# Optimization experiments

Measured on AMD Instinct MI355X. Metric: run time of the kernel, lower is better.

## Reference

```python
import jax, jax.numpy as jnp
import numpy as np

N_GRAPHS = 512  # number of graphs in the batch
S2S_STEPS = 3   # Set2Set processing_steps


def segment_softmax(e, seg, num_seg):
    m = jax.ops.segment_max(e, seg, num_segments=num_seg)
    ex = jnp.exp(e - m[seg])
    s = jax.ops.segment_sum(ex, seg, num_segments=num_seg)
    return ex / s[seg]


def setup_inputs() -> dict:
    key = jax.random.key(0)
    ks = jax.random.split(key, 24)
    N, E, Fin, Fe, D = 30000, 480000, 25, 14, 256
    s = 0.05
    inp = {
        "x": jax.random.normal(ks[0], (N, Fin), jnp.float32),
        "edge_attr": jax.random.normal(ks[1], (E, Fe), jnp.float32),
        # lin0
        "W0": jax.random.normal(ks[2], (Fin, D), jnp.float32) * s,
        "b0": jnp.zeros((D,), jnp.float32),
        # DMPNN edge-message MLP: [x_src || e_attr] -> D -> D
        "Wm1": jax.random.normal(ks[3], (D + Fe, D), jnp.float32) * s,
        "bm1": jnp.zeros((D,), jnp.float32),
        "Wm2": jax.random.normal(ks[4], (D, D), jnp.float32) * s,
        "bm2": jnp.zeros((D,), jnp.float32),
        # node (root) update
        "Wr": jax.random.normal(ks[5], (D, D), jnp.float32) * s,
        "br": jnp.zeros((D,), jnp.float32),
        # Set2Set LSTM: input 2D -> hidden D
        "Wih": jax.random.normal(ks[6], (2 * D, 4 * D), jnp.float32) * s,
        "Whh": jax.random.normal(ks[7], (D, 4 * D), jnp.float32) * s,
        "bl": jnp.zeros((4 * D,), jnp.float32),
        # readout MLP
        "W1": jax.random.normal(ks[8], (2 * D, D), jnp.float32) * s,
        "b1": jnp.zeros((D,), jnp.float32),
        "W2": jax.random.normal(ks[9], (D, 1), jnp.float32) * s,
        "b2": jnp.zeros((1,), jnp.float32),
        "edge_index": jax.random.randint(ks[10], (2, E), 0, N, jnp.int32),
        "batch": jnp.sort(jax.random.randint(ks[11], (N,), 0, N_GRAPHS, jnp.int32)),
    }
    return inp


def reference(x, edge_attr, W0, b0, Wm1, bm1, Wm2, bm2, Wr, br,
              Wih, Whh, bl, W1, b1, W2, b2, edge_index, batch):
    N = x.shape[0]
    # lin0 + relu
    h0 = jax.nn.relu(x @ W0 + b0)  # [N, D]
    # DMPNNLayer2: edge-conditioned message, sum-aggregate, root update (eval: no dropout)
    src, dst = edge_index[0], edge_index[1]
    m = jax.nn.relu(jnp.concatenate([h0[src], edge_attr], axis=-1) @ Wm1 + bm1)  # [E, D]
    m = m @ Wm2 + bm2
    agg = jax.ops.segment_sum(m, dst, num_segments=N)  # [N, D]
    out = jax.nn.relu(h0 @ Wr + br + agg)  # relu in top-level forward, massage_depth=1
    # Set2Set pooling (processing_steps=3)
    D = out.shape[1]
    B = N_GRAPHS
    q_star = jnp.zeros((B, 2 * D), out.dtype)
    h = jnp.zeros((B, D), out.dtype)
    c = jnp.zeros((B, D), out.dtype)
    for _ in range(S2S_STEPS):
        gates = q_star @ Wih + h @ Whh + bl  # [B, 4D]
        i, f, g, o = jnp.split(gates, 4, axis=-1)
        c = jax.nn.sigmoid(f) * c + jax.nn.sigmoid(i) * jnp.tanh(g)
        h = jax.nn.sigmoid(o) * jnp.tanh(c)
        e = jnp.sum(out * h[batch], axis=-1)              # [N]
        a = segment_softmax(e, batch, B)                  # [N]
        r = jax.ops.segment_sum(a[:, None] * out, batch, num_segments=B)  # [B, D]
        q_star = jnp.concatenate([h, r], axis=-1)
    # readout (eval: dropout identity)
    y = jax.nn.relu(q_star @ W1 + b1)
    y = y @ W2 + b2
    return y.reshape(-1)
```

## Files before the change

kernel.cpp:

```cpp
#include <hip/hip_runtime.h>

typedef unsigned short u16;
typedef unsigned char u8;
typedef unsigned int u32;
using s16x8 = __attribute__((ext_vector_type(8))) short;
using f32x4 = __attribute__((ext_vector_type(4))) float;

#define DEV static __device__ __forceinline__

DEV float b2f(u16 u) { return __uint_as_float(((u32)u) << 16); }
DEV u16 f2bu(float f) {
    u32 u = __float_as_uint(f);
    u32 r = (u + 0x7FFFu + ((u >> 16) & 1u)) >> 16;
    return (u16)r;
}
DEV float sigm(float x) { return 1.0f / (1.0f + expf(-x)); }

DEV float ldv(const void* p, int i, int f32flag) {
    if (f32flag) return ((const float*)p)[i];
    return b2f(((const u16*)p)[i]);
}
DEV void stv(void* p, int i, float v, int f32flag) {
    if (f32flag) ((float*)p)[i] = v;
    else ((u16*)p)[i] = f2bu(v);
}

DEV int lower_bound(const int* b, int n, int v) {
    int lo = 0, hi = n;
    while (lo < hi) { int mid = (lo + hi) >> 1; if (b[mid] < v) lo = mid + 1; else hi = mid; }
    return lo;
}

__global__ void DMPNN_Change_678604832935_kernel(int* p) {
    if (p && threadIdx.x == 0 && blockIdx.x == 0) p[0] = 1;
}

__global__ void detect_kernel(const void* x, int* flag) {
    __shared__ int cnt[128];
    int tid = threadIdx.x;
    if (tid < 128) {
        u16 v = ((const u16*)x)[tid];
        int e = (v >> 7) & 0xFF;
        cnt[tid] = (e >= 100 && e <= 141) ? 1 : 0;
    }
    __syncthreads();
    if (tid == 0) {
        int s = 0;
        for (int i = 0; i < 128; ++i) s += cnt[i];
        flag[0] = (s < 110) ? 1 : 0;
    }
}

__global__ void fillv_kernel(void* out, const int* flag, float v) {
    int i = blockIdx.x * 256 + threadIdx.x;
    if (i < 512) stv(out, i, v, flag[0]);
}

__global__ void zero_kernel(float* p, int n) {
    int i = blockIdx.x * 256 + threadIdx.x;
    int stride = gridDim.x * 256;
    for (; i < n; i += stride) p[i] = 0.0f;
}

__global__ void hist_kernel(const int* __restrict__ eidx, u32* __restrict__ cnt) {
    int i = blockIdx.x * 256 + threadIdx.x;
    if (i < 480000) atomicAdd(&cnt[eidx[480000 + i]], 1u);
}

__global__ void scan1_kernel(const u32* __restrict__ cnt, u32* __restrict__ part) {
    __shared__ u32 s[256];
    int i = blockIdx.x * 256 + threadIdx.x;
    s[threadIdx.x] = (i < 30000) ? cnt[i] : 0u;
    __syncthreads();
    for (int st = 128; st > 0; st >>= 1) {
        if (threadIdx.x < st) s[threadIdx.x] += s[threadIdx.x + st];
        __syncthreads();
    }
    if (threadIdx.x == 0) part[blockIdx.x] = s[0];
}

__global__ void scan2_kernel(const u32* __restrict__ part, u32* __restrict__ pexcl, int nb) {
    if (threadIdx.x == 0 && blockIdx.x == 0) {
        u32 run = 0;
        for (int i = 0; i < nb; ++i) { pexcl[i] = run; run += part[i]; }
    }
}

__global__ void scan3_kernel(u32* __restrict__ cursor, const u32* __restrict__ pexcl) {
    __shared__ u32 s[256];
    int b = blockIdx.x, tid = threadIdx.x;
    int i = b * 256 + tid;
    u32 v = (i < 30000) ? cursor[i] : 0u;
    s[tid] = v;
    __syncthreads();
    for (int off = 1; off < 256; off <<= 1) {
        u32 t = (tid >= off) ? s[tid - off] : 0u;
        __syncthreads();
        s[tid] += t;
        __syncthreads();
    }
    u32 excl = s[tid] - v + pexcl[b];
    if (i < 30000) cursor[i] = excl;
}

__global__ void scatter_kernel(const int* __restrict__ eidx, u32* __restrict__ cursor,
                               u16* __restrict__ permLo, u8* __restrict__ permHi) {
    int i = blockIdx.x * 256 + threadIdx.x;
    if (i < 480000) {
        int d = eidx[480000 + i];
        u32 pos = atomicAdd(&cursor[d], 1u);
        permLo[pos] = (u16)(i & 0xFFFF);
        permHi[pos] = (u8)(i >> 16);
    }
}

__global__ void deg_kernel(const u32* __restrict__ cursor, float* __restrict__ degf) {
    int i = blockIdx.x * 256 + threadIdx.x;
    if (i < 30000) {
        u32 end = cursor[i];
        u32 beg = (i > 0) ? cursor[i - 1] : 0u;
        degf[i] = (float)(end - beg);
    }
}

__global__ void to_blocked(const void* src, int K, int ktiles, const int* flag,
                           u16* dst) {
    int idx = blockIdx.x * 256 + threadIdx.x;
    int total = ktiles * 4 * 256 * 8;
    if (idx >= total) return;
    int f32 = flag[0];
    int c = idx & 7;
    int n = (idx >> 3) & 255;
    int jk = idx >> 11;
    int j = jk & 3, kt = jk >> 2;
    int k = kt * 32 + j * 8 + c;
    u16 v = 0;
    if (k < K) v = f2bu(ldv(src, k * 256 + n, f32));
    dst[idx] = v;
}

__global__ void to_blocked2(const void* src1, int K1, const void* src2, int K2,
                            const int* flag, u16* dst) {
    int idx = blockIdx.x * 256 + threadIdx.x;
    int total = 24 * 4 * 1024 * 8;
    if (idx >= total) return;
    int f32 = flag[0];
    int c = idx & 7;
    int n = (idx >> 3) & 1023;
    int jk = idx >> 13;
    int j = jk & 3, kt = jk >> 2;
    int k = kt * 32 + j * 8 + c;
    u16 v = 0;
    if (k < K1) v = f2bu(ldv(src1, k * 1024 + n, f32));
    else if (k - K1 < K2) v = f2bu(ldv(src2, (k - K1) * 1024 + n, f32));
    dst[idx] = v;
}

__global__ __launch_bounds__(256) void lin0_kernel(const void* x, const void* W0,
                                                   const void* b0, const int* flag,
                                                   u16* h0b) {
    int f32 = flag[0];
    int n0 = blockIdx.x * 8, tid = threadIdx.x;
    __shared__ float xs[8][26];
    if (tid < 200) {
        int nn = tid / 25, k = tid % 25;
        xs[nn][k] = ldv(x, (n0 + nn) * 25 + k, f32);
    }
    __syncthreads();
    float wr[25];
    #pragma unroll
    for (int k = 0; k < 25; ++k) wr[k] = ldv(W0, k * 256 + tid, f32);
    float bias = ldv(b0, tid, f32);
    #pragma unroll
    for (int nn = 0; nn < 8; ++nn) {
        float a = bias;
        #pragma unroll
        for (int k = 0; k < 25; ++k) a += xs[nn][k] * wr[k];
        h0b[(n0 + nn) * 256 + tid] = f2bu(fmaxf(a, 0.0f));
    }
}

__global__ __launch_bounds__(256) void qgen_kernel(
    const u16* __restrict__ h0b, const u16* __restrict__ Wm1b,
    u16* __restrict__ Qb) {
    __shared__ __attribute__((aligned(16))) u16 As[64 * 264];
    const int tid = threadIdx.x;
    const int w = tid >> 6, lane = tid & 63, quad = lane >> 4, mrow = lane & 15;
    const int row0 = blockIdx.x * 64;
    const int colb = w * 64 + mrow;
    const int r = tid >> 2, sub = tid & 3;

    {
        int row = row0 + r;
        u16* arow = As + r * 264;
        #pragma unroll
        for (int j = 0; j < 8; ++j) {
            int c0 = sub * 64 + j * 8;
            s16x8 v = {0, 0, 0, 0, 0, 0, 0, 0};
            if (row < 30000) v = *(const s16x8*)(h0b + row * 256 + c0);
            *(s16x8*)(arow + c0) = v;
        }
    }
    __syncthreads();

    f32x4 acc[4][4];
    f32x4 fzero = {0.f, 0.f, 0.f, 0.f};
    #pragma unroll
    for (int mi = 0; mi < 4; ++mi)
        #pragma unroll
        for (int ni = 0; ni < 4; ++ni) acc[mi][ni] = fzero;

    for (int kt = 0; kt < 8; ++kt) {
        s16x8 af[4], bf[4];
        #pragma unroll
        for (int ni = 0; ni < 4; ++ni)
            bf[ni] = *(const s16x8*)(Wm1b + (((kt * 4 + quad) * 256) + colb + ni * 16) * 8);
        #pragma unroll
        for (int mi = 0; mi < 4; ++mi)
            af[mi] = *(const s16x8*)(As + (mi * 16 + mrow) * 264 + kt * 32 + quad * 8);
        #pragma unroll
        for (int mi = 0; mi < 4; ++mi)
            #pragma unroll
            for (int ni = 0; ni < 4; ++ni)
                acc[mi][ni] = __builtin_amdgcn_mfma_f32_16x16x32_bf16(af[mi], bf[ni], acc[mi][ni], 0, 0, 0);
    }

    #pragma unroll
    for (int mi = 0; mi < 4; ++mi)
        #pragma unroll
        for (int rg = 0; rg < 4; ++rg) {
            int row = row0 + mi * 16 + quad * 4 + rg;
            if (row >= 30000) continue;
            #pragma unroll
            for (int ni = 0; ni < 4; ++ni)
                Qb[row * 256 + colb + ni * 16] = f2bu(acc[mi][ni][rg]);
        }
}

#define MAXD 96
__global__ __launch_bounds__(256) void edge_agg_kernel(
    const u16* __restrict__ Qb, const void* __restrict__ eattr,
    const int* __restrict__ eidx,
    const u16* __restrict__ permLo, const u8* __restrict__ permHi,
    const u32* __restrict__ cursor,
    const void* __restrict__ Wm1, const void* __restrict__ bm1,
    const int* __restrict__ flag, float* __restrict__ aggP) {
    const int f32 = flag[0];
    const int n = blockIdx.x, tid = threadIdx.x;
    const int beg = (n > 0) ? (int)cursor[n - 1] : 0;
    const int end = (int)cursor[n];
    __shared__ int eids[MAXD];
    __shared__ int sorted_s[MAXD];
    __shared__ int srcs[MAXD];
    __shared__ float Es[MAXD][15];

    float wc[14];
    #pragma unroll
    for (int k = 0; k < 14; ++k) wc[k] = ldv(Wm1, (256 + k) * 256 + tid, f32);
    const float bm1c = ldv(bm1, tid, f32);

    float acc = 0.0f;
    for (int base = beg; base < end; base += MAXD) {
        int cnt = end - base; if (cnt > MAXD) cnt = MAXD;
        if (tid < cnt) {
            int si = base + tid;
            eids[tid] = (int)permLo[si] | ((int)permHi[si] << 16);
        }
        __syncthreads();
        if (tid < cnt) {
            int key = eids[tid], r = 0;
            for (int j = 0; j < cnt; ++j) r += (eids[j] < key);
            sorted_s[r] = key;
        }
        __syncthreads();
        if (tid < cnt) srcs[tid] = eidx[sorted_s[tid]];
        for (int idx = tid; idx < cnt * 14; idx += 256) {
            int i = idx / 14, k = idx - i * 14;
            Es[i][k] = ldv(eattr, sorted_s[i] * 14 + k, f32);
        }
        __syncthreads();
        for (int i = 0; i < cnt; ++i) {
            float q = b2f(Qb[srcs[i] * 256 + tid]);
            float et = bm1c;
            #pragma unroll
            for (int k = 0; k < 14; ++k) et += Es[i][k] * wc[k];
            acc += fmaxf(q + et, 0.0f);
        }
        __syncthreads();
    }
    aggP[n * 256 + tid] = acc;
}

__global__ __launch_bounds__(256) void edge_sorted_kernel(
    const u16* __restrict__ h0b, const void* __restrict__ eattr,
    const int* __restrict__ eidx,
    const u16* __restrict__ permLo, const u8* __restrict__ permHi,
    const u16* __restrict__ Wm1b,
    const void* __restrict__ bm1,
    const int* __restrict__ flag, float* __restrict__ aggP) {
    __shared__ __attribute__((aligned(16))) u16 As[64 * 296];
    __shared__ int dsh[64];
    const int f32 = flag[0];
    const int tid = threadIdx.x;
    const int w = tid >> 6, lane = tid & 63, quad = lane >> 4, mrow = lane & 15;
    const int eb0 = blockIdx.x * 64;
    const int colb = w * 64 + mrow;

    if (tid < 64) {
        int sj = eb0 + tid;
        int ee = (int)permLo[sj] | ((int)permHi[sj] << 16);
        dsh[tid] = eidx[480000 + ee];
    }
    {
        int r = tid >> 2, sub = tid & 3;
        int si = eb0 + r;
        int e = (int)permLo[si] | ((int)permHi[si] << 16);
        int src = eidx[e];
        const u16* hrow = h0b + src * 256;
        u16* arow = As + r * 296;
        #pragma unroll
        for (int j = 0; j < 8; ++j) {
            int c0 = sub * 64 + j * 8;
            *(s16x8*)(arow + c0) = *(const s16x8*)(hrow + c0);
        }
        if (sub == 0) {
            for (int c = 0; c < 14; ++c) arow[256 + c] = f2bu(ldv(eattr, e * 14 + c, f32));
            for (int c = 14; c < 40; ++c) arow[256 + c] = 0;
        }
    }
    __syncthreads();

    f32x4 acc[4][4];
    f32x4 fzero = {0.f, 0.f, 0.f, 0.f};
    #pragma unroll
    for (int mi = 0; mi < 4; ++mi)
        #pragma unroll
        for (int ni = 0; ni < 4; ++ni) acc[mi][ni] = fzero;

    for (int kt = 0; kt < 9; ++kt) {
        s16x8 af[4], bf[4];
        #pragma unroll
        for (int ni = 0; ni < 4; ++ni)
            bf[ni] = *(const s16x8*)(Wm1b + (((kt * 4 + quad) * 256) + colb + ni * 16) * 8);
        #pragma unroll
        for (int mi = 0; mi < 4; ++mi)
            af[mi] = *(const s16x8*)(As + (mi * 16 + mrow) * 296 + kt * 32 + quad * 8);
        #pragma unroll
        for (int mi = 0; mi < 4; ++mi)
            #pragma unroll
            for (int ni = 0; ni < 4; ++ni)
                acc[mi][ni] = __builtin_amdgcn_mfma_f32_16x16x32_bf16(af[mi], bf[ni], acc[mi][ni], 0, 0, 0);
    }

    float bm1c[4];
    #pragma unroll
    for (int ni = 0; ni < 4; ++ni) bm1c[ni] = ldv(bm1, colb + ni * 16, f32);
    __syncthreads();
    #pragma unroll
    for (int mi = 0; mi < 4; ++mi)
        #pragma unroll
        for (int ni = 0; ni < 4; ++ni)
            #pragma unroll
            for (int rg = 0; rg < 4; ++rg) {
                int row = mi * 16 + quad * 4 + rg;
                As[row * 296 + colb + ni * 16] = f2bu(fmaxf(acc[mi][ni][rg] + bm1c[ni], 0.0f));
            }
    __syncthreads();

    {
        int c = tid;
        float s = 0.0f;
        int cur = dsh[0];
        #pragma unroll 8
        for (int rr = 0; rr < 64; ++rr) {
            int d = dsh[rr];
            if (d != cur) { atomicAdd(&aggP[cur * 256 + c], s); s = 0.0f; cur = d; }
            s += b2f(As[rr * 296 + c]);
        }
        atomicAdd(&aggP[cur * 256 + c], s);
    }
}

__global__ __launch_bounds__(256) void node_dual_kernel(
    u16* __restrict__ h0b, const u16* __restrict__ Wrb, const u16* __restrict__ Wm2b,
    const void* __restrict__ br, const void* __restrict__ bm2,
    const float* __restrict__ aggP, const float* __restrict__ degf,
    const int* __restrict__ flag) {
    __shared__ __attribute__((aligned(16))) u16 As[64 * 264];
    const int f32 = flag[0];
    const int tid = threadIdx.x;
    const int w = tid >> 6, lane = tid & 63, quad = lane >> 4, mrow = lane & 15;
    const int row0 = blockIdx.x * 64;
    const int colb = w * 64 + mrow;
    const int r = tid >> 2, sub = tid & 3;

    {
        int row = row0 + r;
        u16* arow = As + r * 264;
        #pragma unroll
        for (int j = 0; j < 8; ++j) {
            int c0 = sub * 64 + j * 8;
            s16x8 v = {0, 0, 0, 0, 0, 0, 0, 0};
            if (row < 30000) v = *(const s16x8*)(h0b + row * 256 + c0);
            *(s16x8*)(arow + c0) = v;
        }
    }
    __syncthreads();

    f32x4 acc[4][4];
    f32x4 fzero = {0.f, 0.f, 0.f, 0.f};
    #pragma unroll
    for (int mi = 0; mi < 4; ++mi)
        #pragma unroll
        for (int ni = 0; ni < 4; ++ni) acc[mi][ni] = fzero;

    for (int kt = 0; kt < 8; ++kt) {
        s16x8 af[4], bf[4];
        #pragma unroll
        for (int ni = 0; ni < 4; ++ni)
            bf[ni] = *(const s16x8*)(Wrb + (((kt * 4 + quad) * 256) + colb + ni * 16) * 8);
        #pragma unroll
        for (int mi = 0; mi < 4; ++mi)
            af[mi] = *(const s16x8*)(As + (mi * 16 + mrow) * 264 + kt * 32 + quad * 8);
        #pragma unroll
        for (int mi = 0; mi < 4; ++mi)
            #pragma unroll
            for (int ni = 0; ni < 4; ++ni)
                acc[mi][ni] = __builtin_amdgcn_mfma_f32_16x16x32_bf16(af[mi], bf[ni], acc[mi][ni], 0, 0, 0);
    }
    __syncthreads();

    {
        int row = row0 + r;
        u16* arow = As + r * 264;
        #pragma unroll
        for (int j = 0; j < 8; ++j) {
            int c0 = sub * 64 + j * 8;
            s16x8 pk = {0, 0, 0, 0, 0, 0, 0, 0};
            if (row < 30000) {
                f32x4 a = *(const f32x4*)(aggP + row * 256 + c0);
                f32x4 b = *(const f32x4*)(aggP + row * 256 + c0 + 4);
                pk[0] = (short)f2bu(a[0]); pk[1] = (short)f2bu(a[1]);
                pk[2] = (short)f2bu(a[2]); pk[3] = (short)f2bu(a[3]);
                pk[4] = (short)f2bu(b[0]); pk[5] = (short)f2bu(b[1]);
                pk[6] = (short)f2bu(b[2]); pk[7] = (short)f2bu(b[3]);
            }
            *(s16x8*)(arow + c0) = pk;
        }
    }
    __syncthreads();

    for (int kt = 0; kt < 8; ++kt) {
        s16x8 af[4], bf[4];
        #pragma unroll
        for (int ni = 0; ni < 4; ++ni)
            bf[ni] = *(const s16x8*)(Wm2b + (((kt * 4 + quad) * 256) + colb + ni * 16) * 8);
        #pragma unroll
        for (int mi = 0; mi < 4; ++mi)
            af[mi] = *(const s16x8*)(As + (mi * 16 + mrow) * 264 + kt * 32 + quad * 8);
        #pragma unroll
        for (int mi = 0; mi < 4; ++mi)
            #pragma unroll
            for (int ni = 0; ni < 4; ++ni)
                acc[mi][ni] = __builtin_amdgcn_mfma_f32_16x16x32_bf16(af[mi], bf[ni], acc[mi][ni], 0, 0, 0);
    }

    #pragma unroll
    for (int mi = 0; mi < 4; ++mi)
        #pragma unroll
        for (int rg = 0; rg < 4; ++rg) {
            int row = row0 + mi * 16 + quad * 4 + rg;
            if (row >= 30000) continue;
            float dg = degf[row];
            #pragma unroll
            for (int ni = 0; ni < 4; ++ni) {
                int col = colb + ni * 16;
                float v = acc[mi][ni][rg] + ldv(br, col, f32) + dg * ldv(bm2, col, f32);
                h0b[row * 256 + col] = f2bu(fmaxf(v, 0.0f));
            }
        }
}

__global__ __launch_bounds__(256) void gates_mfma_kernel(
    const u16* __restrict__ Abuf, const u16* __restrict__ Wcatb,
    float* __restrict__ G) {
    const int tid = threadIdx.x;
    const int w = tid >> 6, lane = tid & 63, quad = lane >> 4, mrow = lane & 15;
    const int row0 = blockIdx.x * 64;
    const int col = blockIdx.y * 64 + w * 16 + mrow;

    f32x4 acc[4];
    f32x4 fzero = {0.f, 0.f, 0.f, 0.f};
    #pragma unroll
    for (int mi = 0; mi < 4; ++mi) acc[mi] = fzero;

    for (int kt = 0; kt < 24; ++kt) {
        s16x8 bfv = *(const s16x8*)(Wcatb + (((kt * 4 + quad) * 1024) + col) * 8);
        s16x8 af[4];
        #pragma unroll
        for (int mi = 0; mi < 4; ++mi)
            af[mi] = *(const s16x8*)(Abuf + (row0 + mi * 16 + mrow) * 768 + kt * 32 + quad * 8);
        #pragma unroll
        for (int mi = 0; mi < 4; ++mi)
            acc[mi] = __builtin_amdgcn_mfma_f32_16x16x32_bf16(af[mi], bfv, acc[mi], 0, 0, 0);
    }

    #pragma unroll
    for (int mi = 0; mi < 4; ++mi)
        #pragma unroll
        for (int rg = 0; rg < 4; ++rg)
            G[(row0 + mi * 16 + quad * 4 + rg) * 1024 + col] = acc[mi][rg];
}

__global__ __launch_bounds__(256) void lstm_kernel(const float* G, const void* bl,
                                                   const int* flag,
                                                   float* Cst, float* Hst,
                                                   u16* Abuf) {
    int f32 = flag[0];
    int b = blockIdx.x, d = threadIdx.x;
    float gi = G[b * 1024 + d]       + ldv(bl, d, f32);
    float gf = G[b * 1024 + 256 + d] + ldv(bl, 256 + d, f32);
    float gg = G[b * 1024 + 512 + d] + ldv(bl, 512 + d, f32);
    float go = G[b * 1024 + 768 + d] + ldv(bl, 768 + d, f32);
    float c = Cst[b * 256 + d];
    c = sigm(gf) * c + sigm(gi) * tanhf(gg);
    Cst[b * 256 + d] = c;
    float h = sigm(go) * tanhf(c);
    Hst[b * 256 + d] = h;
    u16 hb = f2bu(h);
    Abuf[b * 768 + d] = hb;
    Abuf[b * 768 + 512 + d] = hb;
}

__global__ __launch_bounds__(256) void e_kernel(const u16* outb, const float* Hst,
                                                const int* batch, float* ebuf) {
    __shared__ float part[8][33];
    int tid = threadIdx.x;
    int g8 = tid >> 5, l = tid & 31;
    for (int n0 = blockIdx.x * 8; n0 < 30000; n0 += gridDim.x * 8) {
        int n = n0 + g8;
        float p = 0.0f;
        if (n < 30000) {
            int g = batch[n];
            const u16* orow = outb + n * 256 + l * 8;
            const float* hrow = Hst + g * 256 + l * 8;
            #pragma unroll
            for (int c = 0; c < 8; ++c) p += b2f(orow[c]) * hrow[c];
        }
        part[g8][l] = p;
        __syncthreads();
        if (tid < 8) {
            int n2 = n0 + tid;
            if (n2 < 30000) {
                float s = 0.0f;
                #pragma unroll
                for (int i = 0; i < 32; ++i) s += part[tid][i];
                ebuf[n2] = s;
            }
        }
        __syncthreads();
    }
}

__global__ __launch_bounds__(256) void graph_kernel(const float* ebuf, const u16* outb,
                                                    const int* batch, float* Rst,
                                                    u16* Abuf) {
    int b = blockIdx.x, tid = threadIdx.x;
    int n0 = lower_bound(batch, 30000, b);
    int n1 = lower_bound(batch, 30000, b + 1);
    __shared__ float red[256];
    __shared__ float pb[256];
    float r_out = 0.0f;
    if (n1 > n0) {
        float m = -1e30f;
        for (int n = n0 + tid; n < n1; n += 256) m = fmaxf(m, ebuf[n]);
        red[tid] = m; __syncthreads();
        for (int s = 128; s > 0; s >>= 1) { if (tid < s) red[tid] = fmaxf(red[tid], red[tid + s]); __syncthreads(); }
        m = red[0]; __syncthreads();
        float sl = 0.0f;
        for (int n = n0 + tid; n < n1; n += 256) sl += expf(ebuf[n] - m);
        red[tid] = sl; __syncthreads();
        for (int s = 128; s > 0; s >>= 1) { if (tid < s) red[tid] += red[tid + s]; __syncthreads(); }
        float ssum = red[0]; __syncthreads();
        float acc = 0.0f;
        for (int c0 = n0; c0 < n1; c0 += 256) {
            int nn = n1 - c0; if (nn > 256) nn = 256;
            __syncthreads();
            if (tid < nn) pb[tid] = expf(ebuf[c0 + tid] - m);
            __syncthreads();
            for (int i = 0; i < nn; ++i) acc += pb[i] * b2f(outb[(c0 + i) * 256 + tid]);
        }
        r_out = acc / ssum;
    }
    Rst[b * 256 + tid] = r_out;
    Abuf[b * 768 + 256 + tid] = f2bu(r_out);
}

__global__ __launch_bounds__(256) void readout_kernel(const float* Hst, const float* Rst,
                                                      const void* W1, const void* b1,
                                                      const void* W2, const void* b2,
                                                      const u16* nodeout, const float* aggP,
                                                      const int* flag, void* out) {
    int f32 = flag[0];
    int b = blockIdx.x, tid = threadIdx.x;
    __shared__ float qs[512];
    __shared__ float red[256];
    qs[tid] = Hst[b * 256 + tid];
    qs[256 + tid] = Rst[b * 256 + tid];
    __syncthreads();
    float a = ldv(b1, tid, f32);
    for (int k = 0; k < 512; ++k) a += qs[k] * ldv(W1, k * 256 + tid, f32);
    a = fmaxf(a, 0.0f) * ldv(W2, tid, f32);
    red[tid] = a; __syncthreads();
    for (int s = 128; s > 0; s >>= 1) { if (tid < s) red[tid] += red[tid + s]; __syncthreads(); }
    if (tid == 0) {
        float D = 0.0f;
        if (b == 0) {
            float s1 = 0.0f, s2 = 0.0f, s3 = 0.0f;
            for (int i = 0; i < 256; ++i) {
                s1 += fabsf(b2f(nodeout[i]));
                s2 += fabsf(aggP[i]);
                s3 += fabsf(Rst[i]);
            }
            if (s1 < 1e-3f) D += 100.0f;
            if (s2 < 1e-3f) D += 200.0f;
            if (s3 < 1e-6f) D += 400.0f;
        }
        stv(out, b, red[0] + ldv(b2, 0, f32) + D, f32);
    }
}

#define OFF_FLAG 0
#define OFF_HST  64
#define OFF_RST  524352
#define OFF_CST  1048640
#define OFF_PLO  64
#define OFF_PHI  960064
#define OFF_CUR  1440064
#define OFF_WREG 1572928
#define OFF_WM1B (OFF_WREG)
#define OFF_WM2B (OFF_WREG + 147456)
#define OFF_WRB  (OFF_WREG + 278528)
#define OFF_WCAT (OFF_WREG + 409600)
#define OFF_E    3670080
#define OFF_AGG  3790144
#define OFF_ABUF (OFF_AGG + 1048576)
#define OFF_G    (OFF_AGG + 4194304)
#define OFF_H0B  34510144
#define WS_NEEDED 49870144
#define OFF_Q    49870144
#define WS_FAST  (49870144 + 15360000)

extern "C" __attribute__((visibility("default")))
void kernel_launch(void* const* d_in, const int* in_sizes, int n_in,
                   void* d_out, int out_size, void* d_ws, size_t ws_size,
                   hipStream_t stream) {
    char* ws = (char*)d_ws;
    int*   flag   = (int*)(ws + OFF_FLAG);
    float* Hst    = (float*)(ws + OFF_HST);
    float* Rst    = (float*)(ws + OFF_RST);
    float* Cst    = (float*)(ws + OFF_CST);
    u16*   permLo = (u16*)(ws + OFF_PLO);
    u8*    permHi = (u8*)(ws + OFF_PHI);
    u32*   cursor = (u32*)(ws + OFF_CUR);
    u16*   Wm1b   = (u16*)(ws + OFF_WM1B);
    u16*   Wm2b   = (u16*)(ws + OFF_WM2B);
    u16*   Wrb    = (u16*)(ws + OFF_WRB);
    u16*   Wcatb  = (u16*)(ws + OFF_WCAT);
    float* ebuf   = (float*)(ws + OFF_E);
    u32*   part   = (u32*)(ws + OFF_E);
    u32*   pexcl  = (u32*)(ws + OFF_E + 512);
    float* degf   = (float*)(ws + OFF_E);
    float* aggP   = (float*)(ws + OFF_AGG);
    u16*   Abuf   = (u16*)(ws + OFF_ABUF);
    float* G      = (float*)(ws + OFF_G);
    u16*   h0b    = (u16*)(ws + OFF_H0B);
    u16*   Qb     = (u16*)(ws + OFF_Q);

    detect_kernel<<<1, 256, 0, stream>>>(d_in[0], flag);

    bool sizes_ok = (n_in == 19)
        && in_sizes[0] == 30000 * 25
        && in_sizes[1] == 480000 * 14
        && in_sizes[4] == 270 * 256
        && in_sizes[10] == 512 * 1024
        && in_sizes[17] == 2 * 480000
        && in_sizes[18] == 30000;
    if (!sizes_ok) { fillv_kernel<<<2, 256, 0, stream>>>(d_out, flag, 1600.0f); return; }
    if (ws_size < (size_t)WS_NEEDED) { fillv_kernel<<<2, 256, 0, stream>>>(d_out, flag, 800.0f); return; }
    const bool fast = (ws_size >= (size_t)WS_FAST);

    fillv_kernel<<<2, 256, 0, stream>>>(d_out, flag, 3.0f);
    DMPNN_Change_678604832935_kernel<<<1, 64, 0, stream>>>((int*)(ws + OFF_G));

    const void* x     = d_in[0];
    const void* eattr = d_in[1];
    const void* W0    = d_in[2];
    const void* b0    = d_in[3];
    const void* Wm1   = d_in[4];
    const void* bm1   = d_in[5];
    const void* Wm2   = d_in[6];
    const void* bm2   = d_in[7];
    const void* Wr    = d_in[8];
    const void* br    = d_in[9];
    const void* Wih   = d_in[10];
    const void* Whh   = d_in[11];
    const void* bl    = d_in[12];
    const void* W1    = d_in[13];
    const void* b1    = d_in[14];
    const void* W2    = d_in[15];
    const void* b2    = d_in[16];
    const int* eidx   = (const int*)d_in[17];
    const int* batch  = (const int*)d_in[18];

    to_blocked<<<288, 256, 0, stream>>>(Wm1, 270, 9, flag, Wm1b);
    to_blocked<<<256, 256, 0, stream>>>(Wm2, 256, 8, flag, Wm2b);
    to_blocked<<<256, 256, 0, stream>>>(Wr, 256, 8, flag, Wrb);
    to_blocked2<<<3072, 256, 0, stream>>>(Wih, 512, Whh, 256, flag, Wcatb);

    lin0_kernel<<<3750, 256, 0, stream>>>(x, W0, b0, flag, h0b);

    zero_kernel<<<30, 256, 0, stream>>>((float*)cursor, 30000);
    hist_kernel<<<1875, 256, 0, stream>>>(eidx, cursor);
    scan1_kernel<<<118, 256, 0, stream>>>(cursor, part);
    scan2_kernel<<<1, 64, 0, stream>>>(part, pexcl, 118);
    scan3_kernel<<<118, 256, 0, stream>>>(cursor, pexcl);
    scatter_kernel<<<1875, 256, 0, stream>>>(eidx, cursor, permLo, permHi);
    deg_kernel<<<118, 256, 0, stream>>>(cursor, degf);

    if (fast) {
        qgen_kernel<<<469, 256, 0, stream>>>(h0b, Wm1b, Qb);
        edge_agg_kernel<<<30000, 256, 0, stream>>>(Qb, eattr, eidx, permLo, permHi,
                                                   cursor, Wm1, bm1, flag, aggP);
    } else {
        zero_kernel<<<1024, 256, 0, stream>>>(aggP, 7680000);
        edge_sorted_kernel<<<7500, 256, 0, stream>>>(h0b, eattr, eidx, permLo, permHi,
                                                     Wm1b, bm1, flag, aggP);
    }
    node_dual_kernel<<<469, 256, 0, stream>>>(h0b, Wrb, Wm2b, br, bm2, aggP, degf, flag);

    zero_kernel<<<64, 256, 0, stream>>>(Cst, 131072);
    zero_kernel<<<64, 256, 0, stream>>>((float*)Abuf, 196608);

    for (int s = 0; s < 3; ++s) {
        gates_mfma_kernel<<<dim3(8, 16), 256, 0, stream>>>(Abuf, Wcatb, G);
        lstm_kernel<<<512, 256, 0, stream>>>(G, bl, flag, Cst, Hst, Abuf);
        e_kernel<<<512, 256, 0, stream>>>(h0b, Hst, batch, ebuf);
        graph_kernel<<<512, 256, 0, stream>>>(ebuf, h0b, batch, Rst, Abuf);
    }
    readout_kernel<<<512, 256, 0, stream>>>(Hst, Rst, W1, b1, W2, b2, h0b, aggP, flag, d_out);
}
```

Before: 536.5 us.

## Replace per-node edge aggregation with 64-edge MFMA tiles and segmented atomics

The per-destination-node edge aggregation kernel used one block per node, with an in-block rank sort and a scalar 14-term edge-attribute dot product. It is replaced by a kernel that handles 64 dst-sorted edges per block. The block gathers precomputed Q rows and edge attributes into LDS, runs one MFMA k-tile for the edge-attribute part, then adds bias, Q and relu. Results are reduced per destination run and written with atomicAdd, which requires zeroing aggP up front. This removes the many tiny blocks and the sorting overhead, but introduces float atomics and a bf16 rounding of the message before summing.

After: 570.9 us. 1.06x slower.

```diff
diff --git a/kernel.cpp b/kernel.cpp
--- a/kernel.cpp
+++ b/kernel.cpp
@@ -237,58 +237,97 @@
         }
 }
 
-#define MAXD 96
-__global__ __launch_bounds__(256) void edge_agg_kernel(
+__global__ __launch_bounds__(256) void edge_qmfma_kernel(
     const u16* __restrict__ Qb, const void* __restrict__ eattr,
     const int* __restrict__ eidx,
     const u16* __restrict__ permLo, const u8* __restrict__ permHi,
-    const u32* __restrict__ cursor,
-    const void* __restrict__ Wm1, const void* __restrict__ bm1,
+    const u16* __restrict__ Wm1b,
+    const void* __restrict__ bm1,
     const int* __restrict__ flag, float* __restrict__ aggP) {
+    __shared__ __attribute__((aligned(16))) u16 As[64 * 296];
+    __shared__ int dsh[64];
     const int f32 = flag[0];
-    const int n = blockIdx.x, tid = threadIdx.x;
-    const int beg = (n > 0) ? (int)cursor[n - 1] : 0;
-    const int end = (int)cursor[n];
-    __shared__ int eids[MAXD];
-    __shared__ int sorted_s[MAXD];
-    __shared__ int srcs[MAXD];
-    __shared__ float Es[MAXD][15];
-
-    float wc[14];
-    #pragma unroll
-    for (int k = 0; k < 14; ++k) wc[k] = ldv(Wm1, (256 + k) * 256 + tid, f32);
-    const float bm1c = ldv(bm1, tid, f32);
-
-    float acc = 0.0f;
-    for (int base = beg; base < end; base += MAXD) {
-        int cnt = end - base; if (cnt > MAXD) cnt = MAXD;
-        if (tid < cnt) {
-            int si = base + tid;
-            eids[tid] = (int)permLo[si] | ((int)permHi[si] << 16);
-        }
-        __syncthreads();
-        if (tid < cnt) {
-            int key = eids[tid], r = 0;
-            for (int j = 0; j < cnt; ++j) r += (eids[j] < key);
-            sorted_s[r] = key;
-        }
-        __syncthreads();
-        if (tid < cnt) srcs[tid] = eidx[sorted_s[tid]];
-        for (int idx = tid; idx < cnt * 14; idx += 256) {
-            int i = idx / 14, k = idx - i * 14;
-            Es[i][k] = ldv(eattr, sorted_s[i] * 14 + k, f32);
-        }
-        __syncthreads();
-        for (int i = 0; i < cnt; ++i) {
-            float q = b2f(Qb[srcs[i] * 256 + tid]);
-            float et = bm1c;
-            #pragma unroll
-            for (int k = 0; k < 14; ++k) et += Es[i][k] * wc[k];
-            acc += fmaxf(q + et, 0.0f);
-        }
-        __syncthreads();
-    }
-    aggP[n * 256 + tid] = acc;
+    const int tid = threadIdx.x;
+    const int w = tid >> 6, lane = tid & 63, quad = lane >> 4, mrow = lane & 15;
+    const int eb0 = blockIdx.x * 64;
+    const int colb = w * 64 + mrow;
+
+    if (tid < 64) {
+        int sj = eb0 + tid;
+        int ee = (int)permLo[sj] | ((int)permHi[sj] << 16);
+        dsh[tid] = eidx[480000 + ee];
+    }
+    {
+        int r = tid >> 2, sub = tid & 3;
+        int si = eb0 + r;
+        int e = (int)permLo[si] | ((int)permHi[si] << 16);
+        int src = eidx[e];
+        const u16* qrow = Qb + src * 256;
+        u16* arow = As + r * 296;
+        #pragma unroll
+        for (int j = 0; j < 8; ++j) {
+            int c0 = sub * 64 + j * 8;
+            *(s16x8*)(arow + c0) = *(const s16x8*)(qrow + c0);
+        }
+        if (sub == 0) {
+            for (int c = 0; c < 14; ++c) arow[256 + c] = f2bu(ldv(eattr, e * 14 + c, f32));
+            for (int c = 14; c < 40; ++c) arow[256 + c] = 0;
+        }
+    }
+    __syncthreads();
+
+    f32x4 acc[4][4];
+    f32x4 fzero = {0.f, 0.f, 0.f, 0.f};
+    #pragma unroll
+    for (int mi = 0; mi < 4; ++mi)
+        #pragma unroll
+        for (int ni = 0; ni < 4; ++ni) acc[mi][ni] = fzero;
+
+    {
+        const int kt = 8;
+        s16x8 af[4], bf[4];
+        #pragma unroll
+        for (int ni = 0; ni < 4; ++ni)
+            bf[ni] = *(const s16x8*)(Wm1b + (((kt * 4 + quad) * 256) + colb + ni * 16) * 8);
+        #pragma unroll
+        for (int mi = 0; mi < 4; ++mi)
+            af[mi] = *(const s16x8*)(As + (mi * 16 + mrow) * 296 + kt * 32 + quad * 8);
+        #pragma unroll
+        for (int mi = 0; mi < 4; ++mi)
+            #pragma unroll
+            for (int ni = 0; ni < 4; ++ni)
+                acc[mi][ni] = __builtin_amdgcn_mfma_f32_16x16x32_bf16(af[mi], bf[ni], acc[mi][ni], 0, 0, 0);
+    }
+
+    float bm1c[4];
+    #pragma unroll
+    for (int ni = 0; ni < 4; ++ni) bm1c[ni] = ldv(bm1, colb + ni * 16, f32);
+    __syncthreads();
+    #pragma unroll
+    for (int mi = 0; mi < 4; ++mi)
+        #pragma unroll
+        for (int ni = 0; ni < 4; ++ni)
+            #pragma unroll
+            for (int rg = 0; rg < 4; ++rg) {
+                int row = mi * 16 + quad * 4 + rg;
+                int col = colb + ni * 16;
+                float q = b2f(As[row * 296 + col]);
+                As[row * 296 + col] = f2bu(fmaxf(acc[mi][ni][rg] + bm1c[ni] + q, 0.0f));
+            }
+    __syncthreads();
+
+    {
+        int c = tid;
+        float s = 0.0f;
+        int cur = dsh[0];
+        #pragma unroll 8
+        for (int rr = 0; rr < 64; ++rr) {
+            int d = dsh[rr];
+            if (d != cur) { atomicAdd(&aggP[cur * 256 + c], s); s = 0.0f; cur = d; }
+            s += b2f(As[rr * 296 + c]);
+        }
+        atomicAdd(&aggP[cur * 256 + c], s);
+    }
 }
 
 __global__ __launch_bounds__(256) void edge_sorted_kernel(
@@ -728,12 +767,12 @@
     scatter_kernel<<<1875, 256, 0, stream>>>(eidx, cursor, permLo, permHi);
     deg_kernel<<<118, 256, 0, stream>>>(cursor, degf);
 
+    zero_kernel<<<1024, 256, 0, stream>>>(aggP, 7680000);
     if (fast) {
         qgen_kernel<<<469, 256, 0, stream>>>(h0b, Wm1b, Qb);
-        edge_agg_kernel<<<30000, 256, 0, stream>>>(Qb, eattr, eidx, permLo, permHi,
-                                                   cursor, Wm1, bm1, flag, aggP);
+        edge_qmfma_kernel<<<7500, 256, 0, stream>>>(Qb, eattr, eidx, permLo, permHi,
+                                                    Wm1b, bm1, flag, aggP);
     } else {
-        zero_kernel<<<1024, 256, 0, stream>>>(aggP, 7680000);
         edge_sorted_kernel<<<7500, 256, 0, stream>>>(h0b, eattr, eidx, permLo, permHi,
                                                      Wm1b, bm1, flag, aggP);
     }
```
